# Optimization experiments

Measured on AMD Instinct MI355X. Metric: run time of the kernel, lower is better.

The kernel has to match this reference:

```python
import jax, jax.numpy as jnp
import numpy as np
import math

SIZE = 11
PAD = 5
C1 = 0.01 ** 2
C2 = 0.03 ** 2


def gaussian_window():
    # Matches torch __init__: 1D gaussian (sigma=1.5), normalized, outer product,
    # expanded to depthwise weight of shape (3, 1, 11, 11)
    x = np.arange(SIZE, dtype=np.float32)
    g = np.exp(-((x - SIZE // 2) ** 2) / (2.0 * 1.5 ** 2)).astype(np.float32)
    g = g / g.sum()
    w2d = np.outer(g, g).astype(np.float32)  # (11, 11)
    return jnp.asarray(np.broadcast_to(w2d, (3, 1, SIZE, SIZE)).copy())


def depthwise_conv(x, win):
    return jax.lax.conv_general_dilated(
        x, win,
        window_strides=(1, 1),
        padding=[(PAD, PAD), (PAD, PAD)],
        dimension_numbers=('NCHW', 'OIHW', 'NCHW'),
        feature_group_count=3,
    )


def setup_inputs() -> dict:
    key = jax.random.key(0)
    k1, k2 = jax.random.split(key)
    img1 = jax.random.uniform(k1, (16, 3, 512, 512), dtype=jnp.float32)
    img2 = jax.random.uniform(k2, (16, 3, 512, 512), dtype=jnp.float32)
    return {"img1": img1, "img2": img2, "win": gaussian_window()}


def reference(img1, img2, win):
    mu1 = depthwise_conv(img1, win)
    mu2 = depthwise_conv(img2, win)
    mu1_sq = mu1 * mu1
    mu2_sq = mu2 * mu2
    mu1_mu2 = mu1 * mu2
    sig1_sq = depthwise_conv(img1 * img1, win) - mu1_sq
    sig2_sq = depthwise_conv(img2 * img2, win) - mu2_sq
    sig12 = depthwise_conv(img1 * img2, win) - mu1_mu2
    v = ((2.0 * mu1_mu2 + C1) * (2.0 * sig12 + C2)) / (
        (mu1_sq + mu2_sq + C1) * (sig1_sq + sig2_sq + C2))
    return 1.0 - jnp.mean(v)
```

## Files before the change

### kernel.cpp

```cpp
#include <hip/hip_runtime.h>


#define IMG 512
#define NPIX (16LL * 3 * 512 * 512)
#define GX 8
#define GY 2
#define NG 16
#define NBLK (GX * GY * 48)
#define NPART NBLK

typedef short v8s __attribute__((ext_vector_type(8)));
typedef float v4f __attribute__((ext_vector_type(4)));
typedef __bf16 bf2 __attribute__((ext_vector_type(2)));
typedef float f2  __attribute__((ext_vector_type(2)));

static __device__ __forceinline__ int cvtpk2(f2 v) {
    bf2 r = __builtin_convertvector(v, bf2);
    return __builtin_bit_cast(int, r);
}
static __device__ __forceinline__ unsigned f2bf(float f) {
    unsigned u = __float_as_uint(f);
    return (u + 0x7FFFu + ((u >> 16) & 1u)) >> 16;
}

static __device__ __forceinline__ void gload16(const void* g, void* lds) {
    __builtin_amdgcn_global_load_lds(
        (const __attribute__((address_space(1))) void*)g,
        (__attribute__((address_space(3))) void*)lds, 16, 0, 0);
}

template <int N>
static __device__ __forceinline__ void vwait() {
    if constexpr (N == 4) asm volatile("s_waitcnt vmcnt(4)" ::: "memory");
    else                  asm volatile("s_waitcnt vmcnt(0)" ::: "memory");
}
static __device__ __forceinline__ void lwait0() {
    asm volatile("s_waitcnt lgkmcnt(0)" ::: "memory");
    __builtin_amdgcn_sched_barrier(0);
}

static __device__ __forceinline__ void h_rt(
    const float4 (&L)[4], v8s band, char* hw, int lm, int quad, int slot)
{
    const v4f zacc = {0.f, 0.f, 0.f, 0.f};
    const float4 a0 = L[0], a1 = L[1], b0 = L[2], b1 = L[3];
    f2 a0l; a0l.x = a0.x; a0l.y = a0.y;   f2 a0h; a0h.x = a0.z; a0h.y = a0.w;
    f2 a1l; a1l.x = a1.x; a1l.y = a1.y;   f2 a1h; a1h.x = a1.z; a1h.y = a1.w;
    f2 b0l; b0l.x = b0.x; b0l.y = b0.y;   f2 b0h; b0h.x = b0.z; b0h.y = b0.w;
    f2 b1l; b1l.x = b1.x; b1l.y = b1.y;   f2 b1h; b1h.x = b1.z; b1h.y = b1.w;

    v8s A[4]; int4 w;
    w.x = cvtpk2(a0l); w.y = cvtpk2(a0h); w.z = cvtpk2(a1l); w.w = cvtpk2(a1h);
    A[0] = __builtin_bit_cast(v8s, w);
    w.x = cvtpk2(b0l); w.y = cvtpk2(b0h); w.z = cvtpk2(b1l); w.w = cvtpk2(b1h);
    A[1] = __builtin_bit_cast(v8s, w);
    w.x = cvtpk2(__builtin_elementwise_fma(a0l, a0l, b0l * b0l));
    w.y = cvtpk2(__builtin_elementwise_fma(a0h, a0h, b0h * b0h));
    w.z = cvtpk2(__builtin_elementwise_fma(a1l, a1l, b1l * b1l));
    w.w = cvtpk2(__builtin_elementwise_fma(a1h, a1h, b1h * b1h));
    A[2] = __builtin_bit_cast(v8s, w);
    w.x = cvtpk2(a0l * b0l); w.y = cvtpk2(a0h * b0h);
    w.z = cvtpk2(a1l * b1l); w.w = cvtpk2(a1h * b1h);
    A[3] = __builtin_bit_cast(v8s, w);

    const int wsel = ((lm * 64 + (slot * 2 + (quad >> 1)) * 16) ^ ((lm & 7) << 4))
                     + (quad & 1) * 8;
    #pragma unroll
    for (int p = 0; p < 4; ++p) {
        const v4f acc = __builtin_amdgcn_mfma_f32_16x16x32_bf16(A[p], band, zacc, 0, 0, 0);
        int2 w2;
        f2 lo; lo.x = acc[0]; lo.y = acc[1];
        f2 hi; hi.x = acc[2]; hi.y = acc[3];
        w2.x = cvtpk2(lo); w2.y = cvtpk2(hi);
        *(int2*)(hw + p * 1024 + wsel) = w2;
    }
}

static __device__ __forceinline__ void v_t2(
    v8s band, char* hw, int lm, int quad, int o, f2& vsum)
{
    const v4f zacc = {0.f, 0.f, 0.f, 0.f};
    const int rsel = (lm * 64 + (((quad + 2 * o) & 3) * 16)) ^ ((lm & 7) << 4);
    v4f acc[4];
    #pragma unroll
    for (int p = 0; p < 4; ++p) {
        const v8s hf = *(const v8s*)(hw + p * 1024 + rsel);
        acc[p] = __builtin_amdgcn_mfma_f32_16x16x32_bf16(band, hf, zacc, 0, 0, 0);
    }
    const f2 C1v = {1e-4f, 1e-4f};
    const f2 C2v = {9e-4f, 9e-4f};
    const f2 two = {2.f, 2.f};
    #pragma unroll
    for (int h = 0; h < 2; ++h) {
        f2 m1; m1.x = acc[0][2 * h]; m1.y = acc[0][2 * h + 1];
        f2 m2; m2.x = acc[1][2 * h]; m2.y = acc[1][2 * h + 1];
        f2 es; es.x = acc[2][2 * h]; es.y = acc[2][2 * h + 1];
        f2 ex; ex.x = acc[3][2 * h]; ex.y = acc[3][2 * h + 1];
        const f2 m1s = m1 * m1, m2s = m2 * m2, m12 = m1 * m2;
        const f2 sig = es - m1s - m2s;
        const f2 s12 = ex - m12;
        const f2 num = __builtin_elementwise_fma(two, m12, C1v) *
                       __builtin_elementwise_fma(two, s12, C2v);
        const f2 den = (m1s + m2s + C1v) * (sig + C2v);
        f2 r; r.x = __builtin_amdgcn_rcpf(den.x); r.y = __builtin_amdgcn_rcpf(den.y);
        vsum = __builtin_elementwise_fma(num, r, vsum);
    }
}

__global__ __launch_bounds__(256, 3) void ssim_kernel(
    const float* __restrict__ img1,
    const float* __restrict__ img2,
    const float* __restrict__ win,
    float* __restrict__ partial)
{
    __shared__ __align__(16) char hraw[4][4096];
    __shared__ __align__(16) char raw[4][2][4096];

    const int tid  = threadIdx.x;
    const int lane = tid & 63;
    const int wave = tid >> 6;
    const int lm   = lane & 15;
    const int quad = lane >> 4;

    const int bx = blockIdx.x, by = blockIdx.y, z = blockIdx.z;
    const int rowbase = by * (NG * 16);

    float gl = 0.f;
    if (lane < 11) gl = win[55 + lane] * rsqrtf(win[60]);
    v8s band;
    #pragma unroll
    for (int j = 0; j < 8; ++j) {
        const int t  = quad * 8 + j - lm - 3;
        const int tc = ((unsigned)t > 10u) ? 11 : t;
        band[j] = (short)f2bf(__shfl(gl, tc));
    }

    const size_t zoff = (size_t)z * IMG * IMG;
    const char* p1 = (const char*)(img1 + zoff);
    const char* p2 = (const char*)(img2 + zoff);

    const int gct = bx * 4 + wave;
    const bool colOK = (gct > 0) & (gct < 31);
    const int gcol = gct * 16 - 8 + quad * 8;
    const bool cbA  = (unsigned)gcol >= (unsigned)IMG;
    const bool cbB  = (unsigned)(gcol + 4) >= (unsigned)IMG;
    const bool topE = (by == 0), botE = (by == GY - 1);
    char* hw = hraw[wave];

    const int rowoff = lane >> 3;
    int cb = gct * 64 - 32 + (((lane & 7) ^ (rowoff & 7)) << 4);
    cb = cb < 0 ? 0 : (cb > 2032 ? 2032 : cb);
    const int colbyte = cb;
    const int off0 = lm * 128 + (((2 * quad)     ^ (lm & 7)) << 4);
    const int off1 = lm * 128 + (((2 * quad + 1) ^ (lm & 7)) << 4);

    auto issue_g = [&](int k) {
        const int rb = rowbase + k * 16 - 8;
        int r0 = rb + rowoff;      r0 = r0 < 0 ? 0 : (r0 > IMG - 1 ? IMG - 1 : r0);
        int r1 = rb + 8 + rowoff;  r1 = r1 < 0 ? 0 : (r1 > IMG - 1 ? IMG - 1 : r1);
        char* s = &raw[wave][k & 1][0];
        gload16(p1 + (size_t)r0 * 2048 + colbyte, s);
        gload16(p1 + (size_t)r1 * 2048 + colbyte, s + 1024);
        gload16(p2 + (size_t)r0 * 2048 + colbyte, s + 2048);
        gload16(p2 + (size_t)r1 * 2048 + colbyte, s + 3072);
    };
    auto read_g = [&](int k, float4 (&L)[4], bool rowsE) {
        const char* s = &raw[wave][k & 1][0];
        L[0] = *(const float4*)(s + off0);
        L[1] = *(const float4*)(s + off1);
        L[2] = *(const float4*)(s + off0 + 2048);
        L[3] = *(const float4*)(s + off1 + 2048);
        lwait0();
        if (!colOK || rowsE) {
            const int gr = rowbase + k * 16 - 8 + lm;
            const bool rbad = (unsigned)gr >= (unsigned)IMG;
            float4 zz; zz.x = zz.y = zz.z = zz.w = 0.f;
            if (rbad | cbA) { L[0] = zz; L[2] = zz; }
            if (rbad | cbB) { L[1] = zz; L[3] = zz; }
        }
    };

    f2 vsum = {0.f, 0.f};
    float4 L[4];

    issue_g(0); issue_g(1);

    vwait<4>(); read_g(0, L, topE);
    issue_g(2);
    h_rt(L, band, hw, lm, quad, 0);

    #pragma unroll 2
    for (int k = 1; k <= NG - 2; ++k) {
        vwait<4>(); read_g(k, L, false);
        issue_g(k + 2);
        h_rt(L, band, hw, lm, quad, k & 1);
        v_t2(band, hw, lm, quad, k - 1, vsum);
    }

    vwait<4>(); read_g(NG - 1, L, false);
    h_rt(L, band, hw, lm, quad, (NG - 1) & 1);
    v_t2(band, hw, lm, quad, NG - 2, vsum);

    vwait<0>(); read_g(NG, L, botE);
    h_rt(L, band, hw, lm, quad, NG & 1);
    v_t2(band, hw, lm, quad, NG - 1, vsum);

    float vs = vsum.x + vsum.y;
    #pragma unroll
    for (int off = 32; off > 0; off >>= 1)
        vs += __shfl_down(vs, off, 64);
    if (lane == 0) *(float*)&raw[wave][0][0] = vs;
    __syncthreads();
    if (tid == 0) {
        float t = 0.f;
        #pragma unroll
        for (int w = 0; w < 4; ++w) t += *(const float*)&raw[w][0][0];
        partial[(z * GY + by) * GX + bx] = t;
    }
}

__global__ __launch_bounds__(512) void finalize_kernel(
    const float* __restrict__ partial, float* __restrict__ out)
{
    __shared__ float red[8];
    float s = 0.f;
    if (threadIdx.x < NPART / 4) {
        const float4 t = ((const float4*)partial)[threadIdx.x];
        s = (t.x + t.y) + (t.z + t.w);
    }
    #pragma unroll
    for (int off = 32; off > 0; off >>= 1)
        s += __shfl_down(s, off, 64);
    if ((threadIdx.x & 63) == 0) red[threadIdx.x >> 6] = s;
    __syncthreads();
    if (threadIdx.x == 0) {
        float t = 0.f;
        #pragma unroll
        for (int i = 0; i < 8; ++i) t += red[i];
        out[0] = 1.0f - t / (float)NPIX;
    }
}

extern "C" void kernel_launch(void* const* d_in, const int* in_sizes, int n_in,
                              void* d_out, int out_size, void* d_ws, size_t ws_size,
                              hipStream_t stream) {
    const float* img1 = (const float*)d_in[0];
    const float* img2 = (const float*)d_in[1];
    const float* win  = (const float*)d_in[2];
    float* partialb = (float*)d_ws;

    dim3 grid(GX, GY, 48);
    ssim_kernel<<<grid, dim3(256), 0, stream>>>(img1, img2, win, partialb);
    finalize_kernel<<<1, dim3(512), 0, stream>>>(partialb, (float*)d_out);
}
```

Baseline: 130.3 us.

## Share row-slab staging across sixteen waves in 1024-thread blocks

Blocks grow from four waves to sixteen. Each block covers a 256-column by 128-row tile, and all waves cooperatively load one shared LDS slab per 16-row step instead of each wave fetching its own overlapping 32-column strip. This removes the redundant halo loads between neighbouring waves. In exchange it adds block-wide barriers around each slab read and lowers the number of blocks to 384, which could reduce latency hiding and occupancy.

Measured after the change: 130.1 us. About the same (-0.2%).

```diff
diff --git a/kernel.cpp b/kernel.cpp
--- a/kernel.cpp
+++ b/kernel.cpp
@@ -3,11 +3,13 @@
 
 #define IMG 512
 #define NPIX (16LL * 3 * 512 * 512)
-#define GX 8
-#define GY 2
-#define NG 16
-#define NBLK (GX * GY * 48)
+#define GXC 2
+#define GYB 4
+#define NG 8
+#define NBLK (GXC * GYB * 48)
 #define NPART NBLK
+#define SLAB 18432
+#define RSTR 1104
 
 typedef short v8s __attribute__((ext_vector_type(8)));
 typedef float v4f __attribute__((ext_vector_type(4)));
@@ -31,11 +33,16 @@
 
 template <int N>
 static __device__ __forceinline__ void vwait() {
-    if constexpr (N == 4) asm volatile("s_waitcnt vmcnt(4)" ::: "memory");
-    else                  asm volatile("s_waitcnt vmcnt(0)" ::: "memory");
+    if constexpr (N == 3)      asm volatile("s_waitcnt vmcnt(3)" ::: "memory");
+    else if constexpr (N == 2) asm volatile("s_waitcnt vmcnt(2)" ::: "memory");
+    else                       asm volatile("s_waitcnt vmcnt(0)" ::: "memory");
 }
 static __device__ __forceinline__ void lwait0() {
     asm volatile("s_waitcnt lgkmcnt(0)" ::: "memory");
+    __builtin_amdgcn_sched_barrier(0);
+}
+static __device__ __forceinline__ void blockbar() {
+    __builtin_amdgcn_s_barrier();
     __builtin_amdgcn_sched_barrier(0);
 }
 
@@ -107,23 +114,26 @@
     }
 }
 
-__global__ __launch_bounds__(256, 3) void ssim_kernel(
+__global__ __launch_bounds__(1024) void ssim_kernel(
     const float* __restrict__ img1,
     const float* __restrict__ img2,
     const float* __restrict__ win,
     float* __restrict__ partial)
 {
-    __shared__ __align__(16) char hraw[4][4096];
-    __shared__ __align__(16) char raw[4][2][4096];
+    __shared__ __align__(16) char raw[2][2 * SLAB];
+    __shared__ __align__(16) char hraw[16][4096];
 
     const int tid  = threadIdx.x;
     const int lane = tid & 63;
     const int wave = tid >> 6;
     const int lm   = lane & 15;
     const int quad = lane >> 4;
-
-    const int bx = blockIdx.x, by = blockIdx.y, z = blockIdx.z;
-    const int rowbase = by * (NG * 16);
+    const int wuni = __builtin_amdgcn_readfirstlane(wave);
+
+    const int bxc = blockIdx.x;
+    const int byb = blockIdx.y;
+    const int z   = blockIdx.z;
+    const int rowbase = byb * (NG * 16);
 
     float gl = 0.f;
     if (lane < 11) gl = win[55 + lane] * rsqrtf(win[60]);
@@ -139,37 +149,62 @@
     const char* p1 = (const char*)(img1 + zoff);
     const char* p2 = (const char*)(img2 + zoff);
 
-    const int gct = bx * 4 + wave;
-    const bool colOK = (gct > 0) & (gct < 31);
-    const int gcol = gct * 16 - 8 + quad * 8;
-    const bool cbA  = (unsigned)gcol >= (unsigned)IMG;
-    const bool cbB  = (unsigned)(gcol + 4) >= (unsigned)IMG;
-    const bool topE = (by == 0), botE = (by == GY - 1);
+    const int gcol = bxc * 256 + wave * 16 - 8 + quad * 8;
+    const bool cbA = (unsigned)gcol >= (unsigned)IMG;
+    const bool cbB = (unsigned)(gcol + 4) >= (unsigned)IMG;
+    const bool colOK = !((bxc == 0) & (wave == 0)) & !((bxc == 1) & (wave == 15));
+    const bool topE = (byb == 0), botE = (byb == GYB - 1);
     char* hw = hraw[wave];
 
-    const int rowoff = lane >> 3;
-    int cb = gct * 64 - 32 + (((lane & 7) ^ (rowoff & 7)) << 4);
-    cb = cb < 0 ? 0 : (cb > 2032 ? 2032 : cb);
-    const int colbyte = cb;
-    const int off0 = lm * 128 + (((2 * quad)     ^ (lm & 7)) << 4);
-    const int off1 = lm * 128 + (((2 * quad + 1) ^ (lm & 7)) << 4);
+    const bool has3 = (wuni < 4);
+    const char* base0; const char* base1; const char* base2;
+    int ro_0, ro_1, ro_2, dst0, dst1, dst2;
+    {
+        int js0 = 2 * wave, js1 = 2 * wave + 1, js2 = 32 + wave;
+        #define PREP(J, BASE, ROFF, DST)                                     \
+        {                                                                    \
+            const int offT = (J) * 1024 + lane * 16;                         \
+            const int im   = offT >= SLAB;                                   \
+            int off = offT - im * SLAB;                                      \
+            if (off > 17663) off = 17663;                                    \
+            int row = (int)(((unsigned)off * 60788u) >> 26);                 \
+            int colb = off - row * RSTR;                                     \
+            if (colb > 1072) colb = 1072;           \
+            int g = bxc * 1024 - 32 + colb;                                  \
+            g = g < 0 ? 0 : (g > 2032 ? 2032 : g);                           \
+            BASE = (im ? p2 : p1) + g;                                       \
+            ROFF = row;                                                      \
+            DST  = (J) * 1024;                                               \
+        }
+        PREP(js0, base0, ro_0, dst0)
+        PREP(js1, base1, ro_1, dst1)
+        PREP(js2, base2, ro_2, dst2)
+        #undef PREP
+    }
 
     auto issue_g = [&](int k) {
-        const int rb = rowbase + k * 16 - 8;
-        int r0 = rb + rowoff;      r0 = r0 < 0 ? 0 : (r0 > IMG - 1 ? IMG - 1 : r0);
-        int r1 = rb + 8 + rowoff;  r1 = r1 < 0 ? 0 : (r1 > IMG - 1 ? IMG - 1 : r1);
-        char* s = &raw[wave][k & 1][0];
-        gload16(p1 + (size_t)r0 * 2048 + colbyte, s);
-        gload16(p1 + (size_t)r1 * 2048 + colbyte, s + 1024);
-        gload16(p2 + (size_t)r0 * 2048 + colbyte, s + 2048);
-        gload16(p2 + (size_t)r1 * 2048 + colbyte, s + 3072);
+        const int r0 = rowbase + k * 16 - 8;
+        char* slot = &raw[k & 1][0];
+        int r;
+        r = r0 + ro_0; r = r < 0 ? 0 : (r > IMG - 1 ? IMG - 1 : r);
+        gload16(base0 + (size_t)r * 2048, slot + dst0);
+        r = r0 + ro_1; r = r < 0 ? 0 : (r > IMG - 1 ? IMG - 1 : r);
+        gload16(base1 + (size_t)r * 2048, slot + dst1);
+        if (has3) {
+            r = r0 + ro_2; r = r < 0 ? 0 : (r > IMG - 1 ? IMG - 1 : r);
+            gload16(base2 + (size_t)r * 2048, slot + dst2);
+        }
     };
+
+    const int rb0 = wave * 64 + quad * 32;
+    const int ro0 = lm * RSTR + rb0;
+    const int ro1 = ro0 + 16;
     auto read_g = [&](int k, float4 (&L)[4], bool rowsE) {
-        const char* s = &raw[wave][k & 1][0];
-        L[0] = *(const float4*)(s + off0);
-        L[1] = *(const float4*)(s + off1);
-        L[2] = *(const float4*)(s + off0 + 2048);
-        L[3] = *(const float4*)(s + off1 + 2048);
+        const char* s = &raw[k & 1][0];
+        L[0] = *(const float4*)(s + ro0);
+        L[1] = *(const float4*)(s + ro1);
+        L[2] = *(const float4*)(s + SLAB + ro0);
+        L[3] = *(const float4*)(s + SLAB + ro1);
         lwait0();
         if (!colOK || rowsE) {
             const int gr = rowbase + k * 16 - 8 + lm;
@@ -185,23 +220,33 @@
 
     issue_g(0); issue_g(1);
 
-    vwait<4>(); read_g(0, L, topE);
+    if (has3) vwait<3>(); else vwait<2>();
+    blockbar();
+    read_g(0, L, topE);
+    blockbar();
     issue_g(2);
     h_rt(L, band, hw, lm, quad, 0);
 
     #pragma unroll 2
     for (int k = 1; k <= NG - 2; ++k) {
-        vwait<4>(); read_g(k, L, false);
+        if (has3) vwait<3>(); else vwait<2>();
+        blockbar();
+        read_g(k, L, false);
+        blockbar();
         issue_g(k + 2);
         h_rt(L, band, hw, lm, quad, k & 1);
         v_t2(band, hw, lm, quad, k - 1, vsum);
     }
 
-    vwait<4>(); read_g(NG - 1, L, false);
+    if (has3) vwait<3>(); else vwait<2>();
+    blockbar();
+    read_g(NG - 1, L, false);
     h_rt(L, band, hw, lm, quad, (NG - 1) & 1);
     v_t2(band, hw, lm, quad, NG - 2, vsum);
 
-    vwait<0>(); read_g(NG, L, botE);
+    vwait<0>();
+    blockbar();
+    read_g(NG, L, botE);
     h_rt(L, band, hw, lm, quad, NG & 1);
     v_t2(band, hw, lm, quad, NG - 1, vsum);
 
@@ -209,13 +254,13 @@
     #pragma unroll
     for (int off = 32; off > 0; off >>= 1)
         vs += __shfl_down(vs, off, 64);
-    if (lane == 0) *(float*)&raw[wave][0][0] = vs;
+    if (lane == 0) *(float*)&raw[0][wave * 4] = vs;
     __syncthreads();
     if (tid == 0) {
         float t = 0.f;
         #pragma unroll
-        for (int w = 0; w < 4; ++w) t += *(const float*)&raw[w][0][0];
-        partial[(z * GY + by) * GX + bx] = t;
+        for (int w = 0; w < 16; ++w) t += *(const float*)&raw[0][w * 4];
+        partial[(z * GYB + byb) * GXC + bxc] = t;
     }
 }
 
@@ -249,7 +294,7 @@
     const float* win  = (const float*)d_in[2];
     float* partialb = (float*)d_ws;
 
-    dim3 grid(GX, GY, 48);
-    ssim_kernel<<<grid, dim3(256), 0, stream>>>(img1, img2, win, partialb);
+    dim3 grid(GXC, GYB, 48);
+    ssim_kernel<<<grid, dim3(1024), 0, stream>>>(img1, img2, win, partialb);
     finalize_kernel<<<1, dim3(512), 0, stream>>>(partialb, (float*)d_out);
 }
```
